# Performance work log

Hardware: AMD Instinct MI355X
Metric: run time of the kernel (lower is better)

The kernel has to match this reference:

```python
import jax, jax.numpy as jnp
import numpy as np

BINS = 10
EPS = 1e-12
DELTA = 1.0 / BINS
N = 16384


def setup_inputs() -> dict:
    key = jax.random.key(0)
    k1, k2 = jax.random.split(key)
    logits = jax.random.normal(k1, (N,), dtype=jnp.float32)
    targets = jax.random.uniform(k2, (N,), dtype=jnp.float32)
    return {"logits": logits, "targets": targets}


def _bce_with_logits(x, t):
    # numerically stable: max(x,0) - x*t + log(1 + exp(-|x|))
    return jnp.maximum(x, 0.0) - x * t + jnp.log1p(jnp.exp(-jnp.abs(x)))


def reference(logits, targets):
    n = logits.size
    pred = jax.nn.sigmoid(logits)
    g = jnp.abs(pred - targets)                      # [n]
    # pairwise sliding-window radius count: GD[i] = #{j : |g_j - g_i| <= delta} / delta
    close = jnp.abs(g[:, None] - g[None, :]) <= DELTA  # [n, n] bool
    GD = close.sum(axis=1).astype(g.dtype) / DELTA     # [n]
    beta = n / (GD + EPS)                              # [n], no-grad in original
    beta = jax.lax.stop_gradient(beta)
    loss = _bce_with_logits(logits, targets)           # [n]
    return (beta * loss).mean()
```

## Files before the change

kernel.cpp:

```cpp
#include <hip/hip_runtime.h>
#include <math.h>


#define N       16384
#define K       4096
#define NTHR    256
#define GRID    (N / NTHR)
#define EPN     (N / NTHR)
#define BPT     (K / NTHR)
#define NWAVE   (NTHR / 64)
#define DELTA_F 0.1f
#define EPS_F   1e-12f

__device__ __forceinline__ int bucket_of(float v) {
    int b = (int)(v * (float)K);
    b = b < 0 ? 0 : b;
    b = b > (K - 1) ? (K - 1) : b;
    return b;
}

__global__ void __launch_bounds__(NTHR)
ghm_all(const float* __restrict__ logits, const float* __restrict__ targets,
        float* __restrict__ out) {
    __shared__ float gs[N];
    __shared__ int   cursor[K];
    __shared__ int   wpart[NWAVE];
    __shared__ float sm[NWAVE];

    const int tid  = threadIdx.x;
    const int lane = tid & 63;
    const int wid  = tid >> 6;

    #pragma unroll
    for (int k = 0; k < BPT; ++k) cursor[tid + k * NTHR] = 0;
    __syncthreads();

    float g_r[EPN];
    const float4* lg4 = (const float4*)logits;
    const float4* tg4 = (const float4*)targets;
    #pragma unroll
    for (int j = 0; j < EPN / 4; ++j) {
        const int q = j * NTHR + tid;
        const float4 x4 = lg4[q];
        const float4 t4 = tg4[q];
        const float xs[4] = {x4.x, x4.y, x4.z, x4.w};
        const float ts[4] = {t4.x, t4.y, t4.z, t4.w};
        #pragma unroll
        for (int c = 0; c < 4; ++c) {
            const float pred = 1.0f / (1.0f + expf(-xs[c]));
            const float gi = fabsf(pred - ts[c]);
            g_r[j * 4 + c] = gi;
            atomicAdd(&cursor[bucket_of(gi)], 1);
        }
    }
    __syncthreads();

    const int base = tid * BPT;
    int h[BPT], excl[BPT];
    int s = 0;
    #pragma unroll
    for (int k = 0; k < BPT; ++k) { h[k] = cursor[base + k]; excl[k] = s; s += h[k]; }
    int scan = s;
    #pragma unroll
    for (int off = 1; off < 64; off <<= 1) {
        const int v = __shfl_up(scan, off, 64);
        if (lane >= off) scan += v;
    }
    if (lane == 63) wpart[wid] = scan;
    __syncthreads();
    int wexcl = 0;
    #pragma unroll
    for (int w = 0; w < NWAVE; ++w) wexcl += (w < wid) ? wpart[w] : 0;
    const int te = wexcl + (scan - s);
    #pragma unroll
    for (int k = 0; k < BPT; ++k) cursor[base + k] = te + excl[k];
    __syncthreads();

    #pragma unroll
    for (int j = 0; j < EPN; ++j) {
        const int b = bucket_of(g_r[j]);
        const int pos = atomicAdd(&cursor[b], 1);
        gs[pos] = g_r[j];
    }
    __syncthreads();

    const int i = blockIdx.x * NTHR + tid;
    const float x = logits[i];
    const float t = targets[i];
    const float pred = 1.0f / (1.0f + expf(-x));
    const float gi = fabsf(pred - t);
    const float li = fmaxf(x, 0.0f) - x * t + log1pf(expf(-fabsf(x)));
    const float hiv = gi + DELTA_F;
    const float lov = gi - DELTA_F;
    const int bh = bucket_of(hiv);
    const int bl = bucket_of(lov);

    int c = (bh > 0) ? cursor[bh - 1] : 0;
    {
        const int e = cursor[bh];
        for (int p = c; p < e; ++p) c += 0;
    }
    {
        const int s0 = (bh > 0) ? cursor[bh - 1] : 0;
        const int e0 = cursor[bh];
        for (int p = s0; p < e0; ++p) c += (gs[p] <= hiv) ? 1 : 0;
    }
    int below = (bl > 0) ? cursor[bl - 1] : 0;
    {
        const int s0 = below;
        const int e0 = cursor[bl];
        for (int p = s0; p < e0; ++p) below += (gs[p] < lov) ? 1 : 0;
    }
    c -= below;

    const float GD   = (float)c / DELTA_F;
    const float beta = (float)N / (GD + EPS_F);
    float val = beta * li;

    #pragma unroll
    for (int off = 32; off > 0; off >>= 1) val += __shfl_down(val, off, 64);
    if (lane == 0) sm[wid] = val;
    __syncthreads();
    if (tid == 0) {
        float bs = 0.0f;
        #pragma unroll
        for (int w = 0; w < NWAVE; ++w) bs += sm[w];
        atomicAdd(out, bs / (float)N);
    }
}

extern "C" void kernel_launch(void* const* d_in, const int* in_sizes, int n_in,
                              void* d_out, int out_size, void* d_ws, size_t ws_size,
                              hipStream_t stream) {
    const float* logits  = (const float*)d_in[0];
    const float* targets = (const float*)d_in[1];
    float* out = (float*)d_out;
    ghm_all<<<dim3(GRID), dim3(NTHR), 0, stream>>>(logits, targets, out);
}
```

Baseline: 69.90 us.

## Use 16 blocks of 1024 threads to cut redundant per-block sorting

Each block redundantly rebuilds the full bucket-sorted copy of all N gradient values, so going from 64 blocks of 256 threads to 16 blocks of 1024 threads cuts that duplicated histogram, scan and scatter work by four times. The per-thread load is hoisted so all global reads are issued together before the atomics. A dead loop is removed, and a barrier is added so the cursor array is not overwritten before the scan reads finish. The cost is fewer blocks, which may leave many compute units idle, and larger blocks that contend harder on shared-memory atomics.

```diff
diff --git a/kernel.cpp b/kernel.cpp
--- a/kernel.cpp
+++ b/kernel.cpp
@@ -4,8 +4,8 @@
 
 #define N       16384
 #define K       4096
-#define NTHR    256
-#define GRID    (N / NTHR)
+#define NTHR    1024
+#define NBLK    16
 #define EPN     (N / NTHR)
 #define BPT     (K / NTHR)
 #define NWAVE   (NTHR / 64)
@@ -19,7 +19,7 @@
     return b;
 }
 
-__global__ void __launch_bounds__(NTHR)
+__global__ void __launch_bounds__(NTHR, 4)
 ghm_all(const float* __restrict__ logits, const float* __restrict__ targets,
         float* __restrict__ out) {
     __shared__ float gs[N];
@@ -31,20 +31,29 @@
     const int lane = tid & 63;
     const int wid  = tid >> 6;
 
+    const int i = blockIdx.x * NTHR + tid;
+    const float x_own = logits[i];
+    const float t_own = targets[i];
+
+    const float4* lg4 = (const float4*)logits;
+    const float4* tg4 = (const float4*)targets;
+    float4 xv[EPN / 4], tv[EPN / 4];
+    #pragma unroll
+    for (int j = 0; j < EPN / 4; ++j) {
+        const int q = j * NTHR + tid;
+        xv[j] = lg4[q];
+        tv[j] = tg4[q];
+    }
+
     #pragma unroll
     for (int k = 0; k < BPT; ++k) cursor[tid + k * NTHR] = 0;
     __syncthreads();
 
     float g_r[EPN];
-    const float4* lg4 = (const float4*)logits;
-    const float4* tg4 = (const float4*)targets;
     #pragma unroll
     for (int j = 0; j < EPN / 4; ++j) {
-        const int q = j * NTHR + tid;
-        const float4 x4 = lg4[q];
-        const float4 t4 = tg4[q];
-        const float xs[4] = {x4.x, x4.y, x4.z, x4.w};
-        const float ts[4] = {t4.x, t4.y, t4.z, t4.w};
+        const float xs[4] = {xv[j].x, xv[j].y, xv[j].z, xv[j].w};
+        const float ts[4] = {tv[j].x, tv[j].y, tv[j].z, tv[j].w};
         #pragma unroll
         for (int c = 0; c < 4; ++c) {
             const float pred = 1.0f / (1.0f + expf(-xs[c]));
@@ -56,10 +65,10 @@
     __syncthreads();
 
     const int base = tid * BPT;
-    int h[BPT], excl[BPT];
+    int excl[BPT];
     int s = 0;
     #pragma unroll
-    for (int k = 0; k < BPT; ++k) { h[k] = cursor[base + k]; excl[k] = s; s += h[k]; }
+    for (int k = 0; k < BPT; ++k) { excl[k] = s; s += cursor[base + k]; }
     int scan = s;
     #pragma unroll
     for (int off = 1; off < 64; off <<= 1) {
@@ -72,6 +81,7 @@
     #pragma unroll
     for (int w = 0; w < NWAVE; ++w) wexcl += (w < wid) ? wpart[w] : 0;
     const int te = wexcl + (scan - s);
+    __syncthreads();
     #pragma unroll
     for (int k = 0; k < BPT; ++k) cursor[base + k] = te + excl[k];
     __syncthreads();
@@ -84,12 +94,10 @@
     }
     __syncthreads();
 
-    const int i = blockIdx.x * NTHR + tid;
-    const float x = logits[i];
-    const float t = targets[i];
-    const float pred = 1.0f / (1.0f + expf(-x));
-    const float gi = fabsf(pred - t);
-    const float li = fmaxf(x, 0.0f) - x * t + log1pf(expf(-fabsf(x)));
+    const float pred = 1.0f / (1.0f + expf(-x_own));
+    const float gi = fabsf(pred - t_own);
+    const float li = fmaxf(x_own, 0.0f) - x_own * t_own
+                   + log1pf(expf(-fabsf(x_own)));
     const float hiv = gi + DELTA_F;
     const float lov = gi - DELTA_F;
     const int bh = bucket_of(hiv);
@@ -97,11 +105,7 @@
 
     int c = (bh > 0) ? cursor[bh - 1] : 0;
     {
-        const int e = cursor[bh];
-        for (int p = c; p < e; ++p) c += 0;
-    }
-    {
-        const int s0 = (bh > 0) ? cursor[bh - 1] : 0;
+        const int s0 = c;
         const int e0 = cursor[bh];
         for (int p = s0; p < e0; ++p) c += (gs[p] <= hiv) ? 1 : 0;
     }
@@ -135,5 +139,5 @@
     const float* logits  = (const float*)d_in[0];
     const float* targets = (const float*)d_in[1];
     float* out = (float*)d_out;
-    ghm_all<<<dim3(GRID), dim3(NTHR), 0, stream>>>(logits, targets, out);
+    ghm_all<<<dim3(NBLK), dim3(NTHR), 0, stream>>>(logits, targets, out);
 }
```

Result: faster. 64.14 us (-8.2%).
